# Performance work log

Measured on AMD Instinct MI355X. Metric: run time of the kernel, lower is better.

The kernel has to match this reference:

```python
import jax, jax.numpy as jnp
import numpy as np

B, C_FEAT, C_COND, C_KEY, H, W = 4, 256, 256, 32, 64, 64


def setup_inputs() -> dict:
    key = jax.random.key(0)
    ks = jax.random.split(key, 8)
    s = 0.02
    return {
        "features": jax.random.normal(ks[0], (B, C_FEAT, H, W), jnp.float32),
        "conditions": jax.random.normal(ks[1], (B, C_COND, H, W), jnp.float32),
        "Wq": jax.random.normal(ks[2], (C_KEY, C_COND), jnp.float32) * s,
        "bq": jnp.zeros((C_KEY,), jnp.float32),
        "Wk": jax.random.normal(ks[3], (C_KEY, C_FEAT), jnp.float32) * s,
        "bk": jnp.zeros((C_KEY,), jnp.float32),
        "Wv": jax.random.normal(ks[4], (C_FEAT, C_FEAT), jnp.float32) * s,
        "bv": jnp.zeros((C_FEAT,), jnp.float32),
        "gamma": jnp.zeros((1,), jnp.float32),
    }


def reference(features, conditions, Wq, bq, Wk, bk, Wv, bv, gamma):
    b, c, h, w = features.shape
    n = h * w
    feat = features.reshape(b, c, n)            # [B, C, N]
    cond = conditions.reshape(b, cond_c := conditions.shape[1], n)
    # 1x1 convs == per-pixel linear projections
    q = jnp.einsum('kc,bcn->bnk', Wq, cond) + bq          # [B, N, Ck]
    k = jnp.einsum('kc,bcn->bkn', Wk, feat) + bk[:, None]  # [B, Ck, N]
    v = jnp.einsum('oc,bcn->bon', Wv, feat) + bv[:, None]  # [B, C, N]
    energy = jnp.einsum('bik,bkj->bij', q, k)             # [B, N, N]
    attn = jax.nn.softmax(energy, axis=-1)
    out = jnp.einsum('bcj,bij->bci', v, attn)             # [B, C, N]
    out = out.reshape(b, c, h, w)
    return gamma * out + features
```

## Files before the change

kernel.cpp:

```cpp
#include <hip/hip_runtime.h>

typedef __bf16 bf16_t;
typedef __bf16 bf16x2 __attribute__((ext_vector_type(2)));
typedef __bf16 bf16x8 __attribute__((ext_vector_type(8)));
typedef float f32x4 __attribute__((ext_vector_type(4)));
typedef unsigned u32;
typedef unsigned u32x4 __attribute__((ext_vector_type(4)));

#define N_PIX 4096
#define CFEAT 256
#define CKEY 32
#define NBATCH 4

#if __has_builtin(__builtin_amdgcn_exp2f)
#define EXP2(x) __builtin_amdgcn_exp2f(x)
#else
#define EXP2(x) exp2f(x)
#endif

static __device__ __forceinline__ f32x4 mfma16(bf16x8 a, bf16x8 b, f32x4 c) {
    return __builtin_amdgcn_mfma_f32_16x16x32_bf16(a, b, c, 0, 0, 0);
}

static __device__ __forceinline__ void glds16(const void* g, void* l) {
    __builtin_amdgcn_global_load_lds(
        (const __attribute__((address_space(1))) void*)g,
        (__attribute__((address_space(3))) void*)l, 16, 0, 0);
}

static __device__ __forceinline__ u32 pk2(float lo, float hi) {
    bf16x2 t; t[0] = (bf16_t)lo; t[1] = (bf16_t)hi;
    return __builtin_bit_cast(u32, t);
}

static __device__ __forceinline__ void xpose4(u32 &x, u32 &y) {
#if __has_builtin(__builtin_amdgcn_permlane32_swap) && __has_builtin(__builtin_amdgcn_permlane16_swap)
    auto r32 = __builtin_amdgcn_permlane32_swap(x, y, false, false);
    auto r16 = __builtin_amdgcn_permlane16_swap(r32[0], r32[1], false, false);
    x = r16[0]; y = r16[1];
#else
    const int lane = threadIdx.x & 63;
    const int g = lane >> 4, ln = lane & 15;
    const int i0 = ln + ((g & 1) << 5);
    const int i2 = i0 + 16;
    u32 xs0 = (u32)__shfl((int)x, i0), ys0 = (u32)__shfl((int)y, i0);
    u32 xs2 = (u32)__shfl((int)x, i2), ys2 = (u32)__shfl((int)y, i2);
    x = (g < 2) ? xs0 : ys0;
    y = (g < 2) ? xs2 : ys2;
#endif
}

static __device__ __forceinline__ void softmax_tile32(
    const bf16x8 kf[2], bf16x8 qf, bf16x8 ones,
    f32x4 &accsum, bf16x8 &pa0)
{
    f32x4 zero = {0.f, 0.f, 0.f, 0.f};
    f32x4 st[2];
#pragma unroll
    for (int jt = 0; jt < 2; ++jt) st[jt] = mfma16(kf[jt], qf, zero);
    float ex[8];
#pragma unroll
    for (int jt = 0; jt < 2; ++jt)
#pragma unroll
        for (int r = 0; r < 4; ++r) ex[jt * 4 + r] = EXP2(st[jt][r]);
    u32 a0 = pk2(ex[0], ex[1]), a1 = pk2(ex[2], ex[3]);
    u32 b0 = pk2(ex[4], ex[5]), b1 = pk2(ex[6], ex[7]);
    xpose4(a0, b0); xpose4(a1, b1);
    u32x4 w0 = {a0, a1, b0, b1};
    pa0 = __builtin_bit_cast(bf16x8, w0);
    accsum = mfma16(ones, pa0, accsum);
}

__global__ __launch_bounds__(256) void proj_kernel(
    const float* __restrict__ Wq, const float* __restrict__ bq, const float* __restrict__ cond,
    const float* __restrict__ Wk, const float* __restrict__ bk, const float* __restrict__ feat,
    const float* __restrict__ Wv, const float* __restrict__ bv,
    bf16_t* __restrict__ Qt, bf16_t* __restrict__ Kt, bf16_t* __restrict__ Vv)
{
    __shared__ __attribute__((aligned(16))) bf16_t T[64][40];
    const int lane = threadIdx.x & 63, wave = threadIdx.x >> 6;
    const int g = lane >> 4, ln = lane & 15;
    const int bid = blockIdx.x;
    f32x4 zero = {0.f, 0.f, 0.f, 0.f};

    if (bid < 512) {
        const bool isK = (bid >= 256);
        const int idx = bid & 255;
        const int xt = idx & 63;
        const int b  = idx >> 6;
        const float* W    = isK ? Wk : Wq;
        const float* bias = isK ? bk : bq;
        const float* X  = (isK ? feat : cond) + (size_t)b * CFEAT * N_PIX;
        bf16_t*      Yt = (isK ? Kt : Qt) + (size_t)b * N_PIX * CKEY;
        const float qscale = isK ? 1.0f : 1.4426950408889634f;

        const int m_base = (wave & 1) * 16;
        const int n_loc  = (wave >> 1) * 32;
        const int n_base = xt * 64 + n_loc;

        f32x4 acc[2] = {zero, zero};
        for (int k0 = 0; k0 < CFEAT; k0 += 32) {
            bf16x8 a;
            const float* wp = W + (size_t)(m_base + ln) * CFEAT + k0 + g * 8;
#pragma unroll
            for (int j = 0; j < 8; ++j) a[j] = (bf16_t)wp[j];
#pragma unroll
            for (int nt = 0; nt < 2; ++nt) {
                const float* xp = X + (size_t)(k0 + g * 8) * N_PIX + n_base + nt * 16 + ln;
                bf16x8 bfr;
#pragma unroll
                for (int j = 0; j < 8; ++j) bfr[j] = (bf16_t)xp[(size_t)j * N_PIX];
                acc[nt] = mfma16(a, bfr, acc[nt]);
            }
        }
#pragma unroll
        for (int nt = 0; nt < 2; ++nt)
#pragma unroll
            for (int r = 0; r < 4; ++r) {
                const int ck = m_base + g * 4 + r;
                T[n_loc + nt * 16 + ln][ck] = (bf16_t)((acc[nt][r] + bias[ck]) * qscale);
            }
        __syncthreads();
        const int n  = threadIdx.x >> 2;
        const int sg = threadIdx.x & 3;
        bf16x8 row = *(const bf16x8*)&T[n][sg * 8];
        *(bf16x8*)&Yt[(size_t)(xt * 64 + n) * CKEY + sg * 8] = row;
    } else {
        const int idx = bid - 512;
        const int xt = idx & 127;
        const int b  = idx >> 7;
        const int n_base = xt * 32;
        const int c_wave = wave * 64;
        const float* Xb = feat + (size_t)b * CFEAT * N_PIX;
        bf16_t*      Vb = Vv + (size_t)b * CFEAT * N_PIX;

        f32x4 acc[4][2];
#pragma unroll
        for (int mt = 0; mt < 4; ++mt) { acc[mt][0] = zero; acc[mt][1] = zero; }

        for (int k0 = 0; k0 < CFEAT; k0 += 32) {
            bf16x8 bfr[2];
#pragma unroll
            for (int nt = 0; nt < 2; ++nt) {
                const float* xp = Xb + (size_t)(k0 + g * 8) * N_PIX + n_base + nt * 16 + ln;
#pragma unroll
                for (int j = 0; j < 8; ++j) bfr[nt][j] = (bf16_t)xp[(size_t)j * N_PIX];
            }
#pragma unroll
            for (int mt = 0; mt < 4; ++mt) {
                const float* wp = Wv + (size_t)(c_wave + mt * 16 + ln) * CFEAT + k0 + g * 8;
                bf16x8 a;
#pragma unroll
                for (int j = 0; j < 8; ++j) a[j] = (bf16_t)wp[j];
                acc[mt][0] = mfma16(a, bfr[0], acc[mt][0]);
                acc[mt][1] = mfma16(a, bfr[1], acc[mt][1]);
            }
        }
#pragma unroll
        for (int mt = 0; mt < 4; ++mt)
#pragma unroll
            for (int nt = 0; nt < 2; ++nt)
#pragma unroll
                for (int r = 0; r < 4; ++r) {
                    const int m = c_wave + mt * 16 + g * 4 + r;
                    const int n = n_base + nt * 16 + ln;
                    Vb[(size_t)m * N_PIX + n] = (bf16_t)(acc[mt][nt][r] + bv[m]);
                }
    }
}

__global__ __launch_bounds__(256, 2) void pv_kernel(
    const bf16_t* __restrict__ Qt, const bf16_t* __restrict__ Kt,
    const bf16_t* __restrict__ V,
    const float* __restrict__ features, const float* __restrict__ gamma,
    float* __restrict__ out)
{
    __shared__ __attribute__((aligned(16))) bf16_t Vlds[4][8192];
    __shared__ __attribute__((aligned(16))) bf16_t Plds[2][1024];
    __shared__ float Llds[32];

    const int lane = threadIdx.x & 63, wave = threadIdx.x >> 6;
    const int g = lane >> 4, ln = lane & 15;
    const int b = blockIdx.y;
    const int i_base = blockIdx.x * 32;
    const bool sm = (wave < 2);

    const bf16_t* Qb = Qt + (size_t)b * N_PIX * CKEY;
    const bf16_t* Kb = Kt + (size_t)b * N_PIX * CKEY;
    const bf16_t* Vb = V + (size_t)b * CFEAT * N_PIX;

    const bf16_t* vgp[4];
#pragma unroll
    for (int q = 0; q < 4; ++q) {
        const int s = q * 256 + wave * 64 + lane;
        vgp[q] = Vb + (size_t)(s >> 2) * N_PIX + (s & 3) * 8;
    }

#define STAGE(BUF, JOFF)                                                     \
    { _Pragma("unroll") for (int q = 0; q < 4; ++q)                          \
        glds16(vgp[q] + (JOFF), &Vlds[BUF][(q * 256 + wave * 64) * 8]); }

#define LOADK(DST, JQ)                                                       \
    { _Pragma("unroll") for (int jt = 0; jt < 2; ++jt)                       \
        DST[jt] = *(const bf16x8*)&Kb[(size_t)((JQ) + jt * 16 + ln) * CKEY + g * 8]; }

#define PWRITE(SLOT, PA0)                                                    \
    { *(bf16x8*)&Plds[SLOT][(wave * 16 + ln) * 32 + g * 8] = PA0; }

    bf16x8 qf = {};
    if (sm) qf = *(const bf16x8*)&Qb[(size_t)(i_base + wave * 16 + ln) * CKEY + g * 8];

    bf16x8 ones;
#pragma unroll
    for (int j = 0; j < 8; ++j) ones[j] = (bf16_t)1.0f;

    f32x4 zero = {0.f, 0.f, 0.f, 0.f};
    f32x4 acc[4][2];
#pragma unroll
    for (int ct = 0; ct < 4; ++ct) { acc[ct][0] = zero; acc[ct][1] = zero; }
    f32x4 accsum = zero;

    bf16x8 kfA[2], kfB[2];

    if (sm) LOADK(kfA, 0);
    asm volatile("" ::: "memory");
    STAGE(0, 0);
    STAGE(1, 32);
    if (sm) {
        bf16x8 pa0;
        softmax_tile32(kfA, qf, ones, accsum, pa0);
        PWRITE(0, pa0);
        LOADK(kfA, 32);
    }
    __syncthreads();

#define PV_ITER(NN, KU, KN)                                                  \
  {                                                                          \
    const int nn = (NN);                                                     \
    const bf16_t* Vt = &Vlds[nn & 3][0];                                     \
    bf16x8 vf[4];                                                            \
    _Pragma("unroll")                                                        \
    for (int ct = 0; ct < 4; ++ct)                                           \
      vf[ct] = *(const bf16x8*)&Vt[(wave * 64 + ct * 16 + ln) * 32 + g * 8]; \
    const bf16_t* Pr = &Plds[nn & 1][0];                                     \
    bf16x8 pf[2];                                                            \
    _Pragma("unroll")                                                        \
    for (int it = 0; it < 2; ++it)                                           \
      pf[it] = *(const bf16x8*)&Pr[(it * 16 + ln) * 32 + g * 8];             \
    const bool live = (nn < 127);                                            \
    if (sm && live) LOADK(KN, ((nn + 2) & 127) * 32);                        \
    asm volatile("" ::: "memory");   \
    STAGE((nn + 2) & 3, ((nn * 32 + 64) & (N_PIX - 1)));                     \
    if (sm && live) {                                                        \
      bf16x8 pa0;                                                            \
      softmax_tile32(KU, qf, ones, accsum, pa0);                             \
      PWRITE((nn + 1) & 1, pa0);                                             \
    }                                                                        \
    if (sm) { asm volatile("s_waitcnt vmcnt(6)" ::: "memory"); }             \
    else    { asm volatile("s_waitcnt vmcnt(4)" ::: "memory"); }             \
    asm volatile("s_waitcnt lgkmcnt(0)" ::: "memory");                       \
    __builtin_amdgcn_s_barrier();                                            \
    asm volatile("" ::: "memory");                                           \
    __builtin_amdgcn_s_setprio(1);                                           \
    _Pragma("unroll")                                                        \
    for (int ct = 0; ct < 4; ++ct) {                                         \
      acc[ct][0] = mfma16(vf[ct], pf[0], acc[ct][0]);                        \
      acc[ct][1] = mfma16(vf[ct], pf[1], acc[ct][1]);                        \
    }                                                                        \
    __builtin_amdgcn_s_setprio(0);                                           \
  }

    for (int n2 = 0; n2 < 64; ++n2) {
        PV_ITER(2 * n2,     kfA, kfB);
        PV_ITER(2 * n2 + 1, kfB, kfA);
    }
#undef PV_ITER

    if (sm && g == 0) Llds[wave * 16 + ln] = accsum[0];
    __syncthreads();
    const float gam = gamma[0];
    float sc2[2];
#pragma unroll
    for (int it = 0; it < 2; ++it) sc2[it] = gam / Llds[it * 16 + ln];

#pragma unroll
    for (int ct = 0; ct < 4; ++ct)
#pragma unroll
        for (int it = 0; it < 2; ++it)
#pragma unroll
            for (int r = 0; r < 4; ++r) {
                const int c = wave * 64 + ct * 16 + g * 4 + r;
                const int i = i_base + it * 16 + ln;
                const size_t idx = ((size_t)b * CFEAT + c) * N_PIX + i;
                out[idx] = sc2[it] * acc[ct][it][r] + features[idx];
            }
#undef STAGE
#undef LOADK
#undef PWRITE
}

extern "C" void kernel_launch(void* const* d_in, const int* in_sizes, int n_in,
                              void* d_out, int out_size, void* d_ws, size_t ws_size,
                              hipStream_t stream) {
    const float* features   = (const float*)d_in[0];
    const float* conditions = (const float*)d_in[1];
    const float* Wq  = (const float*)d_in[2];
    const float* bq  = (const float*)d_in[3];
    const float* Wk  = (const float*)d_in[4];
    const float* bk  = (const float*)d_in[5];
    const float* Wv  = (const float*)d_in[6];
    const float* bv  = (const float*)d_in[7];
    const float* gam = (const float*)d_in[8];
    float* out = (float*)d_out;

    bf16_t* Qt = (bf16_t*)d_ws;
    bf16_t* Kt = Qt + (size_t)NBATCH * N_PIX * CKEY;
    bf16_t* Vw = Kt + (size_t)NBATCH * N_PIX * CKEY;

    proj_kernel<<<dim3(1024, 1, 1), 256, 0, stream>>>(
        Wq, bq, conditions, Wk, bk, features, Wv, bv, Qt, Kt, Vw);
    pv_kernel<<<dim3(128, NBATCH, 1), 256, 0, stream>>>(
        Qt, Kt, Vw, features, gam, out);
}
```

Before: 191.0 us.

## Widen PV key tile to 64, swizzle LDS, rebalance staging across waves

The attention PV loop now processes 64 keys per iteration instead of 32, so there are half as many barriers and twice the MFMA work between them. V staging drops from a 4-deep to a 2-deep ring of larger buffers. The non-softmax waves issue more of the global-to-LDS copies so the softmax waves carry less load. V and P tiles in LDS use an XOR swizzle to avoid bank conflicts, and the grid is flattened with a remapped block index that interleaves batches. The risks are a shallower prefetch, which exposes more load latency, and higher register pressure from the wider fragments.

```diff
diff --git a/kernel.cpp b/kernel.cpp
--- a/kernel.cpp
+++ b/kernel.cpp
@@ -50,25 +50,31 @@
 #endif
 }
 
-static __device__ __forceinline__ void softmax_tile32(
-    const bf16x8 kf[2], bf16x8 qf, bf16x8 ones,
-    f32x4 &accsum, bf16x8 &pa0)
+static __device__ __forceinline__ void softmax_tile(
+    const bf16x8 kf[4], bf16x8 qf, bf16x8 ones,
+    f32x4 &accsum, bf16x8 &pa0, bf16x8 &pa1)
 {
     f32x4 zero = {0.f, 0.f, 0.f, 0.f};
-    f32x4 st[2];
-#pragma unroll
-    for (int jt = 0; jt < 2; ++jt) st[jt] = mfma16(kf[jt], qf, zero);
-    float ex[8];
-#pragma unroll
-    for (int jt = 0; jt < 2; ++jt)
+    f32x4 st[4];
+#pragma unroll
+    for (int jt = 0; jt < 4; ++jt) st[jt] = mfma16(kf[jt], qf, zero);
+    float ex[16];
+#pragma unroll
+    for (int jt = 0; jt < 4; ++jt)
 #pragma unroll
         for (int r = 0; r < 4; ++r) ex[jt * 4 + r] = EXP2(st[jt][r]);
-    u32 a0 = pk2(ex[0], ex[1]), a1 = pk2(ex[2], ex[3]);
-    u32 b0 = pk2(ex[4], ex[5]), b1 = pk2(ex[6], ex[7]);
+    u32 a0 = pk2(ex[0],  ex[1]),  a1 = pk2(ex[2],  ex[3]);
+    u32 b0 = pk2(ex[4],  ex[5]),  b1 = pk2(ex[6],  ex[7]);
+    u32 c0 = pk2(ex[8],  ex[9]),  c1 = pk2(ex[10], ex[11]);
+    u32 d0 = pk2(ex[12], ex[13]), d1 = pk2(ex[14], ex[15]);
     xpose4(a0, b0); xpose4(a1, b1);
+    xpose4(c0, d0); xpose4(c1, d1);
     u32x4 w0 = {a0, a1, b0, b1};
+    u32x4 w1 = {c0, c1, d0, d1};
     pa0 = __builtin_bit_cast(bf16x8, w0);
+    pa1 = __builtin_bit_cast(bf16x8, w1);
     accsum = mfma16(ones, pa0, accsum);
+    accsum = mfma16(ones, pa1, accsum);
 }
 
 __global__ __launch_bounds__(256) void proj_kernel(
@@ -175,37 +181,50 @@
     const float* __restrict__ features, const float* __restrict__ gamma,
     float* __restrict__ out)
 {
-    __shared__ __attribute__((aligned(16))) bf16_t Vlds[4][8192];
-    __shared__ __attribute__((aligned(16))) bf16_t Plds[2][1024];
+    __shared__ __attribute__((aligned(16))) bf16_t Vlds[2][16384];
+    __shared__ __attribute__((aligned(16))) bf16_t Plds[2][2048];
     __shared__ float Llds[32];
 
     const int lane = threadIdx.x & 63, wave = threadIdx.x >> 6;
     const int g = lane >> 4, ln = lane & 15;
-    const int b = blockIdx.y;
-    const int i_base = blockIdx.x * 32;
+    const int f = blockIdx.x;
+    const int b = (f & 7) >> 1;
+    const int i_tile = (f & 1) + 2 * (f >> 3);
+    const int i_base = i_tile * 32;
     const bool sm = (wave < 2);
 
     const bf16_t* Qb = Qt + (size_t)b * N_PIX * CKEY;
     const bf16_t* Kb = Kt + (size_t)b * N_PIX * CKEY;
     const bf16_t* Vb = V + (size_t)b * CFEAT * N_PIX;
 
-    const bf16_t* vgp[4];
-#pragma unroll
-    for (int q = 0; q < 4; ++q) {
-        const int s = q * 256 + wave * 64 + lane;
-        vgp[q] = Vb + (size_t)(s >> 2) * N_PIX + (s & 3) * 8;
-    }
-
-#define STAGE(BUF, JOFF)                                                     \
-    { _Pragma("unroll") for (int q = 0; q < 4; ++q)                          \
-        glds16(vgp[q] + (JOFF), &Vlds[BUF][(q * 256 + wave * 64) * 8]); }
-
-#define LOADK(DST, JQ)                                                       \
-    { _Pragma("unroll") for (int jt = 0; jt < 2; ++jt)                       \
+    const int nq = sm ? 4 : 12;
+    const int sbase = sm ? (wave * 64 + lane) : (512 + (wave - 2) * 64 + lane);
+    const bf16_t* vgp[12];
+#pragma unroll
+    for (int q = 0; q < 12; ++q) {
+        const int s = sbase + (q < nq ? q : 0) * 128;
+        const int sc = s >> 3, sj = (s & 7) ^ (sc & 7);
+        vgp[q] = Vb + (size_t)sc * N_PIX + sj * 8;
+    }
+
+#define STAGE(BUF, JOFF)                                                      \
+    if (sm) {                                                                 \
+        _Pragma("unroll") for (int q = 0; q < 4; ++q)                         \
+            glds16(vgp[q] + (JOFF), &Vlds[BUF][(sbase + q * 128) * 8]);       \
+    } else {                                                                  \
+        _Pragma("unroll") for (int q = 0; q < 12; ++q)                        \
+            glds16(vgp[q] + (JOFF), &Vlds[BUF][(sbase + q * 128) * 8]);       \
+    }
+
+#define LOADK(DST, JQ)                                                        \
+    { _Pragma("unroll") for (int jt = 0; jt < 4; ++jt)                        \
         DST[jt] = *(const bf16x8*)&Kb[(size_t)((JQ) + jt * 16 + ln) * CKEY + g * 8]; }
 
-#define PWRITE(SLOT, PA0)                                                    \
-    { *(bf16x8*)&Plds[SLOT][(wave * 16 + ln) * 32 + g * 8] = PA0; }
+#define PWRITE(SLOT, PA0, PA1)                                                \
+    { const int ir = wave * 16 + ln;                                          \
+      char* Pw = (char*)&Plds[SLOT][0] + ir * 128;                            \
+      *(bf16x8*)(Pw + ((g)     ^ (ir & 7)) * 16) = PA0;                       \
+      *(bf16x8*)(Pw + ((4 + g) ^ (ir & 7)) * 16) = PA1; }
 
     bf16x8 qf = {};
     if (sm) qf = *(const bf16x8*)&Qb[(size_t)(i_base + wave * 16 + ln) * CKEY + g * 8];
@@ -220,57 +239,70 @@
     for (int ct = 0; ct < 4; ++ct) { acc[ct][0] = zero; acc[ct][1] = zero; }
     f32x4 accsum = zero;
 
-    bf16x8 kfA[2], kfB[2];
-
-    if (sm) LOADK(kfA, 0);
-    asm volatile("" ::: "memory");
-    STAGE(0, 0);
-    STAGE(1, 32);
-    if (sm) {
-        bf16x8 pa0;
-        softmax_tile32(kfA, qf, ones, accsum, pa0);
-        PWRITE(0, pa0);
-        LOADK(kfA, 32);
-    }
-    __syncthreads();
-
-#define PV_ITER(NN, KU, KN)                                                  \
-  {                                                                          \
-    const int nn = (NN);                                                     \
-    const bf16_t* Vt = &Vlds[nn & 3][0];                                     \
-    bf16x8 vf[4];                                                            \
-    _Pragma("unroll")                                                        \
-    for (int ct = 0; ct < 4; ++ct)                                           \
-      vf[ct] = *(const bf16x8*)&Vt[(wave * 64 + ct * 16 + ln) * 32 + g * 8]; \
-    const bf16_t* Pr = &Plds[nn & 1][0];                                     \
-    bf16x8 pf[2];                                                            \
-    _Pragma("unroll")                                                        \
-    for (int it = 0; it < 2; ++it)                                           \
-      pf[it] = *(const bf16x8*)&Pr[(it * 16 + ln) * 32 + g * 8];             \
-    const bool live = (nn < 127);                                            \
-    if (sm && live) LOADK(KN, ((nn + 2) & 127) * 32);                        \
-    asm volatile("" ::: "memory");   \
-    STAGE((nn + 2) & 3, ((nn * 32 + 64) & (N_PIX - 1)));                     \
-    if (sm && live) {                                                        \
-      bf16x8 pa0;                                                            \
-      softmax_tile32(KU, qf, ones, accsum, pa0);                             \
-      PWRITE((nn + 1) & 1, pa0);                                             \
-    }                                                                        \
-    if (sm) { asm volatile("s_waitcnt vmcnt(6)" ::: "memory"); }             \
-    else    { asm volatile("s_waitcnt vmcnt(4)" ::: "memory"); }             \
-    asm volatile("s_waitcnt lgkmcnt(0)" ::: "memory");                       \
-    __builtin_amdgcn_s_barrier();                                            \
-    asm volatile("" ::: "memory");                                           \
-    __builtin_amdgcn_s_setprio(1);                                           \
-    _Pragma("unroll")                                                        \
-    for (int ct = 0; ct < 4; ++ct) {                                         \
-      acc[ct][0] = mfma16(vf[ct], pf[0], acc[ct][0]);                        \
-      acc[ct][1] = mfma16(vf[ct], pf[1], acc[ct][1]);                        \
-    }                                                                        \
-    __builtin_amdgcn_s_setprio(0);                                           \
+    bf16x8 kfA[4], kfB[4];
+
+    {
+        bf16x8 kf0[4];
+        if (sm) LOADK(kf0, 0);
+        asm volatile("" ::: "memory");
+        STAGE(0, 0);
+        if (sm) {
+            bf16x8 pa0, pa1;
+            softmax_tile(kf0, qf, ones, accsum, pa0, pa1);
+            PWRITE(0, pa0, pa1);
+            LOADK(kfA, 64);
+        }
+        asm volatile("s_waitcnt vmcnt(0)" ::: "memory");
+        asm volatile("s_waitcnt lgkmcnt(0)" ::: "memory");
+        __builtin_amdgcn_s_barrier();
+        asm volatile("" ::: "memory");
+    }
+
+#define PV_ITER(NN, KU, KN)                                                   \
+  {                                                                           \
+    const int nn = (NN);                                                      \
+    const bf16_t* Vt = &Vlds[nn & 1][0];                                      \
+    bf16x8 vf[8];                                                             \
+    _Pragma("unroll")                                                         \
+    for (int ct = 0; ct < 4; ++ct)                                            \
+      _Pragma("unroll")                                                       \
+      for (int s = 0; s < 2; ++s) {                                           \
+        const int c = wave * 64 + ct * 16 + ln;                               \
+        vf[ct * 2 + s] = *(const bf16x8*)&Vt[(c * 8 + ((s * 4 + g) ^ (c & 7))) * 8]; \
+      }                                                                       \
+    const char* Pr = (const char*)&Plds[nn & 1][0];                           \
+    bf16x8 pf[4];                                                             \
+    _Pragma("unroll")                                                         \
+    for (int it = 0; it < 2; ++it)                                            \
+      _Pragma("unroll")                                                       \
+      for (int s = 0; s < 2; ++s)                                             \
+        pf[it * 2 + s] = *(const bf16x8*)(Pr + (it * 16 + ln) * 128           \
+                           + ((s * 4 + g) ^ (ln & 7)) * 16);                  \
+    STAGE((nn + 1) & 1, (((nn + 1) & 63) * 64));                              \
+    const bool live = (nn < 63);                                              \
+    if (sm && live) {                                                         \
+      LOADK(KN, ((nn + 2) & 63) * 64);                                        \
+      bf16x8 pa0, pa1;                                                        \
+      softmax_tile(KU, qf, ones, accsum, pa0, pa1);                           \
+      PWRITE((nn + 1) & 1, pa0, pa1);                                         \
+    }                                                                         \
+    if (sm) { asm volatile("s_waitcnt vmcnt(4)" ::: "memory"); }              \
+    else    { asm volatile("s_waitcnt vmcnt(0)" ::: "memory"); }              \
+    asm volatile("s_waitcnt lgkmcnt(0)" ::: "memory");                        \
+    __builtin_amdgcn_s_barrier();                                             \
+    asm volatile("" ::: "memory");                                            \
+    __builtin_amdgcn_s_setprio(1);                                            \
+    _Pragma("unroll")                                                         \
+    for (int ct = 0; ct < 4; ++ct)                                            \
+      _Pragma("unroll")                                                       \
+      for (int it = 0; it < 2; ++it) {                                        \
+        acc[ct][it] = mfma16(vf[ct * 2 + 0], pf[it * 2 + 0], acc[ct][it]);    \
+        acc[ct][it] = mfma16(vf[ct * 2 + 1], pf[it * 2 + 1], acc[ct][it]);    \
+      }                                                                       \
+    __builtin_amdgcn_s_setprio(0);                                            \
   }
 
-    for (int n2 = 0; n2 < 64; ++n2) {
+    for (int n2 = 0; n2 < 32; ++n2) {
         PV_ITER(2 * n2,     kfA, kfB);
         PV_ITER(2 * n2 + 1, kfB, kfA);
     }
@@ -319,6 +351,6 @@
 
     proj_kernel<<<dim3(1024, 1, 1), 256, 0, stream>>>(
         Wq, bq, conditions, Wk, bk, features, Wv, bv, Qt, Kt, Vw);
-    pv_kernel<<<dim3(128, NBATCH, 1), 256, 0, stream>>>(
+    pv_kernel<<<dim3(512, 1, 1), 256, 0, stream>>>(
         Qt, Kt, Vw, features, gam, out);
 }
```

Measured after the change: 173.0 us. -9.4%, faster.
